# Kernel tuning notes

Hardware: AMD Instinct MI355X
Metric: run time of the kernel (lower is better)

The kernel has to match this reference:

```python
import jax, jax.numpy as jnp
import numpy as np

N, C = 32768, 1000


def setup_inputs() -> dict:
    key = jax.random.key(0)
    k1, k2 = jax.random.split(key)
    pred_y = jax.random.normal(k1, (N, C), dtype=jnp.float32)
    true_y = jax.random.randint(k2, (N, C), 0, 2, dtype=jnp.int32)
    return {"pred_y": pred_y, "true_y": true_y}


def reference(pred_y, true_y):
    # Original per-class loss: sum_{i in pos, j in neg} [log(1+exp(-p_i)) + log(1+exp(n_j))] / (|pos|*|neg|)
    # which algebraically equals mean_{i in pos} softplus(-p_i) + mean_{j in neg} softplus(n_j).
    pos = true_y == 1                      # [N, C]
    neg = true_y == 0                      # [N, C]
    n_pos = pos.sum(axis=0).astype(pred_y.dtype)   # [C]
    n_neg = neg.sum(axis=0).astype(pred_y.dtype)   # [C]
    sp_pos = jnp.where(pos, jax.nn.softplus(-pred_y), 0.0).sum(axis=0)  # [C]
    sp_neg = jnp.where(neg, jax.nn.softplus(pred_y), 0.0).sum(axis=0)   # [C]
    # Classes are counted only if both labels present (torch.unique == 2 branch).
    valid = (n_pos > 0) & (n_neg > 0)
    loss_c = sp_pos / jnp.maximum(n_pos, 1.0) + sp_neg / jnp.maximum(n_neg, 1.0)
    n_valid = jnp.maximum(valid.sum().astype(pred_y.dtype), 1.0)
    return jnp.sum(jnp.where(valid, loss_c, 0.0)) / n_valid
```

## Files before the change

### kernel.cpp

```cpp
#include <hip/hip_runtime.h>

#define C_DIM 1000
#define CPAD  1024

typedef float f32x4 __attribute__((ext_vector_type(4)));
typedef int   i32x4 __attribute__((ext_vector_type(4)));

#define GLOAD(dst, addr) \
    asm volatile("global_load_dwordx4 %0, %1, off" : "=v"(dst) : "v"(addr))

__global__ __launch_bounds__(1024) void nrl_partial_kernel(
    const float* __restrict__ pred,
    const int*   __restrict__ labels,
    float*        __restrict__ ws_sp_pos,
    float*        __restrict__ ws_sp_neg,
    unsigned int* __restrict__ ws_cnt,
    int N, int S, int store_mode)
{
    const int g   = threadIdx.x >> 8;
    const int tid = threadIdx.x & 255;

    __shared__ float        s_sp[4][CPAD];
    __shared__ float        s_sn[4][CPAD];
    __shared__ unsigned int s_ct[4][CPAD];

    const float NEG_LOG2E = -1.4426950408889634f;
    const float LN2       =  0.6931471805599453f;

    float l2p[4] = {0.f,0.f,0.f,0.f};
    float l2n[4] = {0.f,0.f,0.f,0.f};
    float lip[4] = {0.f,0.f,0.f,0.f};
    float lin[4] = {0.f,0.f,0.f,0.f};
    unsigned int cnt[4] = {0u,0u,0u,0u};

#define PROC(P, Y)                                                          \
    {                                                                       \
        _Pragma("unroll")                                                   \
        for (int j = 0; j < 4; ++j) {                                       \
            const float x  = (P)[j];                                        \
            const float u  = NEG_LOG2E * fabsf(x);                          \
            const float e2 = __builtin_amdgcn_exp2f(u);                     \
            const float l2 = __builtin_amdgcn_logf(1.0f + e2);              \
            const float r  = fmaxf(x, 0.0f);                                \
            const float rn = r - x;                        \
            const bool isp = ((Y)[j] == 1);                                 \
            l2p[j] += isp ? l2 : 0.0f;                                      \
            l2n[j] += isp ? 0.0f : l2;                                      \
            lip[j] += isp ? rn : 0.0f;                                      \
            lin[j] += isp ? 0.0f : r;                                       \
            cnt[j] += isp ? 1u : 0x10000u;                                  \
        }                                                                   \
    }

    if (tid < 250) {
        const int c0 = tid * 4;
        const int v       = (blockIdx.x << 2) | g;
        const int vstride = gridDim.x << 2;

        int r = v;
        for (; r + 3 * vstride < N; r += 4 * vstride) {
            const size_t b0 = (size_t)r * C_DIM + c0;
            const size_t b1 = (size_t)(r +     vstride) * C_DIM + c0;
            const size_t b2 = (size_t)(r + 2 * vstride) * C_DIM + c0;
            const size_t b3 = (size_t)(r + 3 * vstride) * C_DIM + c0;

            f32x4 p0, p1, p2, p3;
            i32x4 y0, y1, y2, y3;
            GLOAD(p0, pred + b0);   GLOAD(y0, labels + b0);
            GLOAD(p1, pred + b1);   GLOAD(y1, labels + b1);
            GLOAD(p2, pred + b2);   GLOAD(y2, labels + b2);
            GLOAD(p3, pred + b3);   GLOAD(y3, labels + b3);
            asm volatile("s_waitcnt vmcnt(0)" ::: "memory");
            __builtin_amdgcn_sched_barrier(0);
            PROC(p0, y0) PROC(p1, y1) PROC(p2, y2) PROC(p3, y3)
        }
        for (; r < N; r += vstride) {
            const size_t b0 = (size_t)r * C_DIM + c0;
            const f32x4 p0 = *reinterpret_cast<const f32x4*>(pred + b0);
            const i32x4 y0 = *reinterpret_cast<const i32x4*>(labels + b0);
            PROC(p0, y0)
        }
#undef PROC

        float4 vp, vn; uint4 vc;
        vp.x = l2p[0]*LN2 + lip[0]; vp.y = l2p[1]*LN2 + lip[1];
        vp.z = l2p[2]*LN2 + lip[2]; vp.w = l2p[3]*LN2 + lip[3];
        vn.x = l2n[0]*LN2 + lin[0]; vn.y = l2n[1]*LN2 + lin[1];
        vn.z = l2n[2]*LN2 + lin[2]; vn.w = l2n[3]*LN2 + lin[3];
        vc.x = cnt[0]; vc.y = cnt[1]; vc.z = cnt[2]; vc.w = cnt[3];
        *reinterpret_cast<float4*>(&s_sp[g][c0]) = vp;
        *reinterpret_cast<float4*>(&s_sn[g][c0]) = vn;
        *reinterpret_cast<uint4*>(&s_ct[g][c0])  = vc;
    }
    __syncthreads();

    const int t = threadIdx.x;
    if (t < C_DIM) {
        const float sp = s_sp[0][t] + s_sp[1][t] + s_sp[2][t] + s_sp[3][t];
        const float sn = s_sn[0][t] + s_sn[1][t] + s_sn[2][t] + s_sn[3][t];
        const unsigned int c = s_ct[0][t] + s_ct[1][t] + s_ct[2][t] + s_ct[3][t];
        if (store_mode) {
            const size_t off = (size_t)blockIdx.x * CPAD + t;
            ws_sp_pos[off] = sp;
            ws_sp_neg[off] = sn;
            ws_cnt[off]    = c;
        } else {
            const size_t off = (size_t)(blockIdx.x % S) * CPAD + t;
            atomicAdd(&ws_sp_pos[off], sp);
            atomicAdd(&ws_sp_neg[off], sn);
            atomicAdd(&ws_cnt[off],    c);
        }
    }
}

__global__ __launch_bounds__(256) void nrl_reduce_kernel(
    const float*        __restrict__ ws_sp_pos,
    const float*        __restrict__ ws_sp_neg,
    const unsigned int* __restrict__ ws_cnt,
    float* __restrict__ LV, int S)
{
    const int j  = blockIdx.x;
    const int c0 = j * 4;

    float4 a = {0.f,0.f,0.f,0.f};
    float4 b = {0.f,0.f,0.f,0.f};
    uint4  c = {0u,0u,0u,0u};
    for (int s = threadIdx.x; s < S; s += 256) {
        const size_t off = (size_t)s * CPAD + c0;
        const float4 aa = *reinterpret_cast<const float4*>(ws_sp_pos + off);
        const float4 bb = *reinterpret_cast<const float4*>(ws_sp_neg + off);
        const uint4  cc = *reinterpret_cast<const uint4*>(ws_cnt + off);
        a.x += aa.x; a.y += aa.y; a.z += aa.z; a.w += aa.w;
        b.x += bb.x; b.y += bb.y; b.z += bb.z; b.w += bb.w;
        c.x += cc.x; c.y += cc.y; c.z += cc.z; c.w += cc.w;
    }

#pragma unroll
    for (int off = 32; off > 0; off >>= 1) {
        a.x += __shfl_down(a.x, off); a.y += __shfl_down(a.y, off);
        a.z += __shfl_down(a.z, off); a.w += __shfl_down(a.w, off);
        b.x += __shfl_down(b.x, off); b.y += __shfl_down(b.y, off);
        b.z += __shfl_down(b.z, off); b.w += __shfl_down(b.w, off);
        c.x += __shfl_down(c.x, off); c.y += __shfl_down(c.y, off);
        c.z += __shfl_down(c.z, off); c.w += __shfl_down(c.w, off);
    }

    __shared__ float4 w_a[4];
    __shared__ float4 w_b[4];
    __shared__ uint4  w_c[4];
    const int wid  = threadIdx.x >> 6;
    const int lane = threadIdx.x & 63;
    if (lane == 0) { w_a[wid] = a; w_b[wid] = b; w_c[wid] = c; }
    __syncthreads();

    if (threadIdx.x == 0) {
        float sp[4] = {0.f,0.f,0.f,0.f};
        float sn[4] = {0.f,0.f,0.f,0.f};
        unsigned int ct[4] = {0u,0u,0u,0u};
#pragma unroll
        for (int w = 0; w < 4; ++w) {
            sp[0] += w_a[w].x; sp[1] += w_a[w].y; sp[2] += w_a[w].z; sp[3] += w_a[w].w;
            sn[0] += w_b[w].x; sn[1] += w_b[w].y; sn[2] += w_b[w].z; sn[3] += w_b[w].w;
            ct[0] += w_c[w].x; ct[1] += w_c[w].y; ct[2] += w_c[w].z; ct[3] += w_c[w].w;
        }
        float L = 0.f, V = 0.f;
#pragma unroll
        for (int q = 0; q < 4; ++q) {
            const float np = (float)(ct[q] & 0xFFFFu);
            const float nn = (float)(ct[q] >> 16);
            const bool valid = (np > 0.f) && (nn > 0.f);
            const float l = sp[q] / fmaxf(np, 1.f) + sn[q] / fmaxf(nn, 1.f);
            L += valid ? l   : 0.f;
            V += valid ? 1.f : 0.f;
        }
        atomicAdd(&LV[0], L);
        atomicAdd(&LV[1], V);
    }
}

__global__ void nrl_final_kernel(const float* __restrict__ LV,
                                 float* __restrict__ out)
{
    out[0] = LV[0] / fmaxf(LV[1], 1.0f);
}

extern "C" void kernel_launch(void* const* d_in, const int* in_sizes, int n_in,
                              void* d_out, int out_size, void* d_ws, size_t ws_size,
                              hipStream_t stream)
{
    const float* pred   = (const float*)d_in[0];
    const int*   labels = (const int*)d_in[1];
    const int N = in_sizes[0] / C_DIM;

    const size_t bytes512 = 3ull * 512 * CPAD * 4ull + 16;
    const size_t bytes256 = 3ull * 256 * CPAD * 4ull + 16;

    int store_mode, S, nblk;
    if (ws_size >= bytes512) {
        store_mode = 1; S = 512; nblk = 512;
    } else if (ws_size >= bytes256) {
        store_mode = 1; S = 256; nblk = 256;
    } else {
        store_mode = 0; nblk = 256;
        S = (int)((ws_size - 16) / (3ull * CPAD * 4ull));
        if (S > 64) S = 64;
        if (S < 1)  S = 1;
    }

    float*        ws_sp_pos = (float*)d_ws;
    float*        ws_sp_neg = ws_sp_pos + (size_t)S * CPAD;
    unsigned int* ws_cnt    = (unsigned int*)(ws_sp_neg + (size_t)S * CPAD);
    float*        LV        = (float*)(ws_cnt + (size_t)S * CPAD);

    if (store_mode) {
        hipMemsetAsync(LV, 0, 2 * sizeof(float), stream);
    } else {
        hipMemsetAsync(d_ws, 0, 3ull * S * CPAD * 4ull + 2 * sizeof(float), stream);
    }

    nrl_partial_kernel<<<nblk, 1024, 0, stream>>>(pred, labels,
                                                  ws_sp_pos, ws_sp_neg, ws_cnt,
                                                  N, S, store_mode);
    nrl_reduce_kernel<<<250, 256, 0, stream>>>(ws_sp_pos, ws_sp_neg,
                                               ws_cnt, LV, S);
    nrl_final_kernel<<<1, 1, 0, stream>>>(LV, (float*)d_out);
}
```

Measured before the change: 65.53 us.

## Interleave partial sums in workspace and fuse final divide via last-block ticket

Partial sums are now stored interleaved (sp, sn, count per class) in one array, staged through shared memory so each block writes contiguous rows, and the reduce kernel reads three uint4 per row. The final single-thread kernel and the store-mode memset are removed. The last reduce block, chosen through an atomic ticket reset in the partial kernel, sums the per-block results and writes the output. This cuts one launch and one memset, at the cost of extra syncthreads and a ticket-based handoff whose correctness depends on ordering between the two kernels.

```diff
diff --git a/kernel.cpp b/kernel.cpp
--- a/kernel.cpp
+++ b/kernel.cpp
@@ -1,7 +1,8 @@
 #include <hip/hip_runtime.h>
 
 #define C_DIM 1000
-#define CPAD  1024
+#define WPC   3
+#define RSTR  3072
 
 typedef float f32x4 __attribute__((ext_vector_type(4)));
 typedef int   i32x4 __attribute__((ext_vector_type(4)));
@@ -12,17 +13,18 @@
 __global__ __launch_bounds__(1024) void nrl_partial_kernel(
     const float* __restrict__ pred,
     const int*   __restrict__ labels,
-    float*        __restrict__ ws_sp_pos,
-    float*        __restrict__ ws_sp_neg,
-    unsigned int* __restrict__ ws_cnt,
+    unsigned int* __restrict__ ws_data,
+    unsigned int* __restrict__ ticket,
     int N, int S, int store_mode)
 {
     const int g   = threadIdx.x >> 8;
     const int tid = threadIdx.x & 255;
 
-    __shared__ float        s_sp[4][CPAD];
-    __shared__ float        s_sn[4][CPAD];
-    __shared__ unsigned int s_ct[4][CPAD];
+    if (blockIdx.x == 0 && threadIdx.x == 0) atomicExch(ticket, 0u);
+
+    __shared__ float        s_sp[4][1024];
+    __shared__ float        s_sn[4][1024];
+    __shared__ unsigned int s_ct[4][1024];
 
     const float NEG_LOG2E = -1.4426950408889634f;
     const float LN2       =  0.6931471805599453f;
@@ -95,93 +97,122 @@
     __syncthreads();
 
     const int t = threadIdx.x;
+    float sp = 0.f, sn = 0.f;
+    unsigned int c = 0u;
     if (t < C_DIM) {
-        const float sp = s_sp[0][t] + s_sp[1][t] + s_sp[2][t] + s_sp[3][t];
-        const float sn = s_sn[0][t] + s_sn[1][t] + s_sn[2][t] + s_sn[3][t];
-        const unsigned int c = s_ct[0][t] + s_ct[1][t] + s_ct[2][t] + s_ct[3][t];
-        if (store_mode) {
-            const size_t off = (size_t)blockIdx.x * CPAD + t;
-            ws_sp_pos[off] = sp;
-            ws_sp_neg[off] = sn;
-            ws_cnt[off]    = c;
-        } else {
-            const size_t off = (size_t)(blockIdx.x % S) * CPAD + t;
-            atomicAdd(&ws_sp_pos[off], sp);
-            atomicAdd(&ws_sp_neg[off], sn);
-            atomicAdd(&ws_cnt[off],    c);
+        sp = s_sp[0][t] + s_sp[1][t] + s_sp[2][t] + s_sp[3][t];
+        sn = s_sn[0][t] + s_sn[1][t] + s_sn[2][t] + s_sn[3][t];
+        c  = s_ct[0][t] + s_ct[1][t] + s_ct[2][t] + s_ct[3][t];
+    }
+    __syncthreads();
+
+    unsigned int* stage = reinterpret_cast<unsigned int*>(&s_sp[0][0]);
+    if (t < C_DIM) {
+        stage[3*t + 0] = __float_as_uint(sp);
+        stage[3*t + 1] = __float_as_uint(sn);
+        stage[3*t + 2] = c;
+    }
+    __syncthreads();
+
+    if (store_mode) {
+        unsigned int* dst = ws_data + (size_t)blockIdx.x * RSTR;
+        for (int w = threadIdx.x; w < WPC * C_DIM; w += 1024)
+            dst[w] = stage[w];
+    } else {
+        unsigned int* dst = ws_data + (size_t)(blockIdx.x % S) * RSTR;
+        for (int w = threadIdx.x; w < WPC * C_DIM; w += 1024) {
+            if ((w % 3) == 2) atomicAdd(&dst[w], stage[w]);
+            else              atomicAdd((float*)&dst[w], __uint_as_float(stage[w]));
         }
     }
 }
 
 __global__ __launch_bounds__(256) void nrl_reduce_kernel(
-    const float*        __restrict__ ws_sp_pos,
-    const float*        __restrict__ ws_sp_neg,
-    const unsigned int* __restrict__ ws_cnt,
-    float* __restrict__ LV, int S)
+    const unsigned int* __restrict__ ws_data,
+    float*        __restrict__ pb,
+    unsigned int* __restrict__ ticket,
+    float* __restrict__ out, int S)
 {
-    const int j  = blockIdx.x;
-    const int c0 = j * 4;
-
-    float4 a = {0.f,0.f,0.f,0.f};
-    float4 b = {0.f,0.f,0.f,0.f};
-    uint4  c = {0u,0u,0u,0u};
+    const int j = blockIdx.x;
+    float sp[4] = {0.f,0.f,0.f,0.f};
+    float sn[4] = {0.f,0.f,0.f,0.f};
+    unsigned int ct[4] = {0u,0u,0u,0u};
+
     for (int s = threadIdx.x; s < S; s += 256) {
-        const size_t off = (size_t)s * CPAD + c0;
-        const float4 aa = *reinterpret_cast<const float4*>(ws_sp_pos + off);
-        const float4 bb = *reinterpret_cast<const float4*>(ws_sp_neg + off);
-        const uint4  cc = *reinterpret_cast<const uint4*>(ws_cnt + off);
-        a.x += aa.x; a.y += aa.y; a.z += aa.z; a.w += aa.w;
-        b.x += bb.x; b.y += bb.y; b.z += bb.z; b.w += bb.w;
-        c.x += cc.x; c.y += cc.y; c.z += cc.z; c.w += cc.w;
+        const unsigned int* row = ws_data + (size_t)s * RSTR + j * 12;
+        const uint4 A = *reinterpret_cast<const uint4*>(row + 0);
+        const uint4 B = *reinterpret_cast<const uint4*>(row + 4);
+        const uint4 C = *reinterpret_cast<const uint4*>(row + 8);
+        sp[0] += __uint_as_float(A.x); sn[0] += __uint_as_float(A.y); ct[0] += A.z;
+        sp[1] += __uint_as_float(A.w); sn[1] += __uint_as_float(B.x); ct[1] += B.y;
+        sp[2] += __uint_as_float(B.z); sn[2] += __uint_as_float(B.w); ct[2] += C.x;
+        sp[3] += __uint_as_float(C.y); sn[3] += __uint_as_float(C.z); ct[3] += C.w;
     }
 
 #pragma unroll
     for (int off = 32; off > 0; off >>= 1) {
-        a.x += __shfl_down(a.x, off); a.y += __shfl_down(a.y, off);
-        a.z += __shfl_down(a.z, off); a.w += __shfl_down(a.w, off);
-        b.x += __shfl_down(b.x, off); b.y += __shfl_down(b.y, off);
-        b.z += __shfl_down(b.z, off); b.w += __shfl_down(b.w, off);
-        c.x += __shfl_down(c.x, off); c.y += __shfl_down(c.y, off);
-        c.z += __shfl_down(c.z, off); c.w += __shfl_down(c.w, off);
-    }
-
-    __shared__ float4 w_a[4];
-    __shared__ float4 w_b[4];
-    __shared__ uint4  w_c[4];
+#pragma unroll
+        for (int q = 0; q < 4; ++q) {
+            sp[q] += __shfl_down(sp[q], off);
+            sn[q] += __shfl_down(sn[q], off);
+            ct[q] += __shfl_down(ct[q], off);
+        }
+    }
+
+    __shared__ float        w_sp[4][4], w_sn[4][4];
+    __shared__ unsigned int w_ct[4][4];
     const int wid  = threadIdx.x >> 6;
     const int lane = threadIdx.x & 63;
-    if (lane == 0) { w_a[wid] = a; w_b[wid] = b; w_c[wid] = c; }
-    __syncthreads();
-
+    if (lane == 0) {
+#pragma unroll
+        for (int q = 0; q < 4; ++q) { w_sp[wid][q]=sp[q]; w_sn[wid][q]=sn[q]; w_ct[wid][q]=ct[q]; }
+    }
+    __syncthreads();
+
+    __shared__ int s_last;
     if (threadIdx.x == 0) {
-        float sp[4] = {0.f,0.f,0.f,0.f};
-        float sn[4] = {0.f,0.f,0.f,0.f};
-        unsigned int ct[4] = {0u,0u,0u,0u};
-#pragma unroll
-        for (int w = 0; w < 4; ++w) {
-            sp[0] += w_a[w].x; sp[1] += w_a[w].y; sp[2] += w_a[w].z; sp[3] += w_a[w].w;
-            sn[0] += w_b[w].x; sn[1] += w_b[w].y; sn[2] += w_b[w].z; sn[3] += w_b[w].w;
-            ct[0] += w_c[w].x; ct[1] += w_c[w].y; ct[2] += w_c[w].z; ct[3] += w_c[w].w;
-        }
         float L = 0.f, V = 0.f;
 #pragma unroll
         for (int q = 0; q < 4; ++q) {
-            const float np = (float)(ct[q] & 0xFFFFu);
-            const float nn = (float)(ct[q] >> 16);
+            float tsp = 0.f, tsn = 0.f; unsigned int tct = 0u;
+#pragma unroll
+            for (int w = 0; w < 4; ++w) { tsp+=w_sp[w][q]; tsn+=w_sn[w][q]; tct+=w_ct[w][q]; }
+            const float np = (float)(tct & 0xFFFFu);
+            const float nn = (float)(tct >> 16);
             const bool valid = (np > 0.f) && (nn > 0.f);
-            const float l = sp[q] / fmaxf(np, 1.f) + sn[q] / fmaxf(nn, 1.f);
+            const float l = tsp / fmaxf(np, 1.f) + tsn / fmaxf(nn, 1.f);
             L += valid ? l   : 0.f;
             V += valid ? 1.f : 0.f;
         }
-        atomicAdd(&LV[0], L);
-        atomicAdd(&LV[1], V);
-    }
-}
-
-__global__ void nrl_final_kernel(const float* __restrict__ LV,
-                                 float* __restrict__ out)
-{
-    out[0] = LV[0] / fmaxf(LV[1], 1.0f);
+        atomicExch(&pb[2*j + 0], L);
+        atomicExch(&pb[2*j + 1], V);
+        __threadfence();
+        const unsigned int old = atomicAdd(ticket, 1u);
+        s_last = (old == (unsigned int)(gridDim.x - 1)) ? 1 : 0;
+    }
+    __syncthreads();
+
+    if (s_last) {
+        const int t = threadIdx.x;
+        float l = 0.f, v = 0.f;
+        if (t < 250) {
+            l = atomicAdd(&pb[2*t + 0], 0.0f);
+            v = atomicAdd(&pb[2*t + 1], 0.0f);
+        }
+#pragma unroll
+        for (int off = 32; off > 0; off >>= 1) {
+            l += __shfl_down(l, off);
+            v += __shfl_down(v, off);
+        }
+        __shared__ float f_l[4], f_v[4];
+        if (lane == 0) { f_l[wid] = l; f_v[wid] = v; }
+        __syncthreads();
+        if (t == 0) {
+            const float L = f_l[0] + f_l[1] + f_l[2] + f_l[3];
+            const float V = f_v[0] + f_v[1] + f_v[2] + f_v[3];
+            out[0] = L / fmaxf(V, 1.0f);
+        }
+    }
 }
 
 extern "C" void kernel_launch(void* const* d_in, const int* in_sizes, int n_in,
@@ -192,8 +223,9 @@
     const int*   labels = (const int*)d_in[1];
     const int N = in_sizes[0] / C_DIM;
 
-    const size_t bytes512 = 3ull * 512 * CPAD * 4ull + 16;
-    const size_t bytes256 = 3ull * 256 * CPAD * 4ull + 16;
+    const size_t tail      = 500 * 4 + 64;
+    const size_t bytes512  = (size_t)512 * RSTR * 4 + tail;
+    const size_t bytes256  = (size_t)256 * RSTR * 4 + tail;
 
     int store_mode, S, nblk;
     if (ws_size >= bytes512) {
@@ -202,26 +234,21 @@
         store_mode = 1; S = 256; nblk = 256;
     } else {
         store_mode = 0; nblk = 256;
-        S = (int)((ws_size - 16) / (3ull * CPAD * 4ull));
+        S = (int)((ws_size - tail) / ((size_t)RSTR * 4));
         if (S > 64) S = 64;
         if (S < 1)  S = 1;
     }
 
-    float*        ws_sp_pos = (float*)d_ws;
-    float*        ws_sp_neg = ws_sp_pos + (size_t)S * CPAD;
-    unsigned int* ws_cnt    = (unsigned int*)(ws_sp_neg + (size_t)S * CPAD);
-    float*        LV        = (float*)(ws_cnt + (size_t)S * CPAD);
-
-    if (store_mode) {
-        hipMemsetAsync(LV, 0, 2 * sizeof(float), stream);
-    } else {
-        hipMemsetAsync(d_ws, 0, 3ull * S * CPAD * 4ull + 2 * sizeof(float), stream);
-    }
-
-    nrl_partial_kernel<<<nblk, 1024, 0, stream>>>(pred, labels,
-                                                  ws_sp_pos, ws_sp_neg, ws_cnt,
+    unsigned int* ws_data = (unsigned int*)d_ws;
+    float*        pb      = (float*)(ws_data + (size_t)S * RSTR);
+    unsigned int* ticket  = (unsigned int*)(pb + 500);
+
+    if (!store_mode) {
+        hipMemsetAsync(ws_data, 0, (size_t)S * RSTR * 4, stream);
+    }
+
+    nrl_partial_kernel<<<nblk, 1024, 0, stream>>>(pred, labels, ws_data, ticket,
                                                   N, S, store_mode);
-    nrl_reduce_kernel<<<250, 256, 0, stream>>>(ws_sp_pos, ws_sp_neg,
-                                               ws_cnt, LV, S);
-    nrl_final_kernel<<<1, 1, 0, stream>>>(LV, (float*)d_out);
+    nrl_reduce_kernel<<<250, 256, 0, stream>>>(ws_data, pb, ticket,
+                                               (float*)d_out, S);
 }
```

Result: faster. 55.88 us (-14.7%).
